# Kernel optimization log

Measured on AMD Instinct MI355X. Metric: run time of the kernel, lower is better.

The kernel has to match this reference:

```python
import jax, jax.numpy as jnp
import numpy as np

GAMMA = 2.0
ALPHA = 0.25
EPS = 1e-4
BETA = 1.0 / 9.0  # smooth-L1 transition point


def _make_boxes(key, shape, img, smin, smax):
    k1, k2 = jax.random.split(key)
    ctr = jax.random.uniform(k1, shape + (2,), minval=0.0, maxval=img)
    wh = jax.random.uniform(k2, shape + (2,), minval=smin, maxval=smax)
    return jnp.concatenate([ctr - 0.5 * wh, ctr + 0.5 * wh], axis=-1)


def setup_inputs() -> dict:
    B, N, C, M = 8, 65536, 80, 64
    key = jax.random.key(0)
    k1, k2, k3, k4, k5 = jax.random.split(key, 5)
    classifications = jax.random.uniform(k1, (B, N, C), minval=0.0, maxval=1.0, dtype=jnp.float32)
    regressions = jax.random.normal(k2, (B, N, 4), dtype=jnp.float32)
    anchors = _make_boxes(k3, (1, N), 512.0, 16.0, 128.0)
    gt_boxes = _make_boxes(k4, (B, M), 512.0, 32.0, 256.0)
    labels = jax.random.randint(k5, (B, M), 0, C).astype(jnp.float32)
    # mark last quarter of annotations as padding (label == -1), keep >=1 valid
    pad = jnp.arange(M) >= (3 * M // 4)
    labels = jnp.where(pad[None, :], -1.0, labels)
    annotations = jnp.concatenate([gt_boxes, labels[..., None]], axis=-1)
    return {"classifications": classifications, "regressions": regressions,
            "anchors": anchors, "annotations": annotations}


def _pairwise_iou(a, b):
    # a: (N,4), b: (M,4) boxes as (x1,y1,x2,y2) -> (N,M)
    area_a = (a[:, 2] - a[:, 0]) * (a[:, 3] - a[:, 1])
    area_b = (b[:, 2] - b[:, 0]) * (b[:, 3] - b[:, 1])
    iw = jnp.clip(jnp.minimum(a[:, None, 2], b[None, :, 2]) - jnp.maximum(a[:, None, 0], b[None, :, 0]), 0.0)
    ih = jnp.clip(jnp.minimum(a[:, None, 3], b[None, :, 3]) - jnp.maximum(a[:, None, 1], b[None, :, 1]), 0.0)
    inter = iw * ih
    ua = jnp.clip(area_a[:, None] + area_b[None, :] - inter, 1e-8)
    return inter / ua


def _focal_loss(classifications, regressions, anchors, annotations):
    anchor = anchors[0]  # (N,4)
    aw = anchor[:, 2] - anchor[:, 0]
    ah = anchor[:, 3] - anchor[:, 1]
    acx = anchor[:, 0] + 0.5 * aw
    acy = anchor[:, 1] + 0.5 * ah
    norm = jnp.array([0.1, 0.1, 0.2, 0.2], dtype=jnp.float32)

    def per_image(cls, reg, ann):
        labels = ann[:, 4]
        valid = labels != -1.0  # (M,)
        cls = jnp.clip(cls, EPS, 1.0 - EPS)  # (N,C)
        iou = _pairwise_iou(anchor, ann[:, :4])  # (N,M)
        iou = jnp.where(valid[None, :], iou, -1.0)  # exclude padded annotations
        iou_max = jnp.max(iou, axis=1)
        iou_argmax = jnp.argmax(iou, axis=1)
        pos = iou_max > 0.5
        neg = iou_max < 0.4
        num_pos = jnp.sum(pos.astype(jnp.float32))
        assigned = ann[iou_argmax]  # (N,5) gather of matched annotation
        one_hot = jax.nn.one_hot(assigned[:, 4].astype(jnp.int32), cls.shape[-1], dtype=cls.dtype)
        # -1 = ignore, 0 = background, one-hot for positives
        targets = jnp.where(pos[:, None], one_hot,
                            jnp.where(neg[:, None], 0.0, -1.0))
        alpha_f = jnp.where(targets == 1.0, ALPHA, 1.0 - ALPHA)
        fw = jnp.where(targets == 1.0, 1.0 - cls, cls)
        fw = alpha_f * fw ** GAMMA
        bce = -(targets * jnp.log(cls) + (1.0 - targets) * jnp.log(1.0 - cls))
        cls_loss = jnp.where(targets == -1.0, 0.0, fw * bce)
        cls_loss = jnp.sum(cls_loss) / jnp.maximum(num_pos, 1.0)
        gw = assigned[:, 2] - assigned[:, 0]
        gh = assigned[:, 3] - assigned[:, 1]
        gcx = assigned[:, 0] + 0.5 * gw
        gcy = assigned[:, 1] + 0.5 * gh
        gw = jnp.clip(gw, 1.0)
        gh = jnp.clip(gh, 1.0)
        t = jnp.stack([(gcx - acx) / aw, (gcy - acy) / ah,
                       jnp.log(gw / aw), jnp.log(gh / ah)], axis=1) / norm
        diff = jnp.abs(t - reg)
        sl1 = jnp.where(diff < BETA, 0.5 * 9.0 * diff ** 2, diff - 0.5 / 9.0)
        sl1 = jnp.where(pos[:, None], sl1, 0.0)
        reg_loss = jnp.where(num_pos > 0,
                             jnp.sum(sl1) / (jnp.maximum(num_pos, 1.0) * 4.0), 0.0)
        return cls_loss, reg_loss

    cls_losses, reg_losses = jax.vmap(per_image)(classifications, regressions, annotations)
    return jnp.mean(cls_losses) + jnp.mean(reg_losses)


def reference(classifications, regressions, anchors, annotations):
    return _focal_loss(classifications, regressions, anchors, annotations)
```

## Files before the change

kernel.cpp:

```cpp
#include <hip/hip_runtime.h>
#include <math.h>

constexpr int B = 8, N = 65536, C = 80, M = 64;
constexpr int APB = 256;
constexpr int BPI = N / APB;
constexpr float F_ALPHA = 0.25f;
constexpr float F_EPS = 1e-4f;
constexpr float F_BETA = 1.0f / 9.0f;
constexpr float K_NEG = 0.75f * 0.6931471805599453f;

__device__ __forceinline__ float waveReduceSum(float v) {
    #pragma unroll
    for (int off = 32; off > 0; off >>= 1) v += __shfl_down(v, off, 64);
    return v;
}

__global__ __launch_bounds__(256) void fused_kernel(
    const float* __restrict__ anchors,
    const float* __restrict__ regs,
    const float* __restrict__ ann,
    const float* __restrict__ cls,
    float4* __restrict__ partials)
{
    const int b = blockIdx.y;
    const int n0 = blockIdx.x * APB;
    const int tid = threadIdx.x;
    const int wave = tid >> 6, lane = tid & 63;

    __shared__ float4 sbox[M];
    __shared__ float  sarea[M];
    __shared__ float  slab[M];
    __shared__ float  slim[APB];
    __shared__ float  swsum[3][4];

    if (tid < M) {
        const float* a = ann + (size_t)(b * M + tid) * 5;
        const float x1 = a[0], y1 = a[1], x2 = a[2], y2 = a[3], lb = a[4];
        sbox[tid] = make_float4(x1, y1, x2, y2);
        sarea[tid] = (lb != -1.0f) ? (x2 - x1) * (y2 - y1) : __builtin_huge_valf();
        slab[tid] = lb;
    }
    __syncthreads();

    const int n = n0 + tid;
    const float4 av = reinterpret_cast<const float4*>(anchors)[n];
    const float aarea = (av.z - av.x) * (av.w - av.y);

    float bn = -1.0f, bd = 0.0f;
    int bestj = 0;
    #pragma unroll 8
    for (int j = 0; j < M; ++j) {
        const float4 bb = sbox[j];
        const float iw = fmaxf(fminf(av.z, bb.z) - fmaxf(av.x, bb.x), 0.0f);
        const float ih = fmaxf(fminf(av.w, bb.w) - fmaxf(av.y, bb.y), 0.0f);
        const float inter = iw * ih;
        const float ua = fmaxf(aarea + sarea[j] - inter, 1e-8f);
        const bool take = inter * bd > bn * ua;
        bn = take ? inter : bn;
        bd = take ? ua : bd;
        bestj = take ? j : bestj;
    }
    const bool pos = bn > 0.5f * bd;
    const bool neg = bn < 0.4f * bd;
    const int code = pos ? (int)slab[bestj] : (neg ? -2 : -1);
    slim[tid] = (pos || neg) ? (1.0f - F_EPS) : 0.0f;

    float np = 0.0f, rl = 0.0f, delta = 0.0f;
    if (pos) {
        np = 1.0f;
        const float4 g = sbox[bestj];
        float gw = g.z - g.x, gh = g.w - g.y;
        const float gcx = g.x + 0.5f * gw, gcy = g.y + 0.5f * gh;
        gw = fmaxf(gw, 1.0f);
        gh = fmaxf(gh, 1.0f);
        const float aw = av.z - av.x, ah = av.w - av.y;
        const float acx = av.x + 0.5f * aw, acy = av.y + 0.5f * ah;
        const float t0 = ((gcx - acx) / aw) / 0.1f;
        const float t1 = ((gcy - acy) / ah) / 0.1f;
        const float t2 = logf(gw / aw) / 0.2f;
        const float t3 = logf(gh / ah) / 0.2f;
        const float4 rv = reinterpret_cast<const float4*>(regs)[(size_t)b * N + n];
        const float d0 = fabsf(t0 - rv.x), d1 = fabsf(t1 - rv.y);
        const float d2 = fabsf(t2 - rv.z), d3 = fabsf(t3 - rv.w);
        auto sl1 = [](float d) { return d < F_BETA ? 4.5f * d * d : d - (0.5f / 9.0f); };
        rl = sl1(d0) + sl1(d1) + sl1(d2) + sl1(d3);

        const float xp = cls[((size_t)b * N + n) * C + code];
        const float x = fminf(fmaxf(xp, F_EPS), 1.0f - F_EPS);
        const float om = 1.0f - x;
        delta = F_ALPHA * om * om * (-__logf(x))
              - (1.0f - F_ALPHA) * x * x * (-__logf(om));
    }

    np = waveReduceSum(np);
    rl = waveReduceSum(rl);
    if (lane == 0) { swsum[0][wave] = np; swsum[1][wave] = rl; }
    __syncthreads();

    const float4* __restrict__ cp =
        reinterpret_cast<const float4*>(cls) + ((size_t)b * N + n0) * (C / 4);
    float a0 = 0.0f, a1 = 0.0f, a2 = 0.0f, a3 = 0.0f;
    #pragma unroll 4
    for (int k = 0; k < APB * C / 4 / 256; ++k) {
        const int f = k * 256 + tid;
        const int nl = f / 20;
        const float lim = slim[nl];
        const float4 v = cp[f];
        const float vv[4] = {v.x, v.y, v.z, v.w};
        float* accp[4] = {&a0, &a1, &a2, &a3};
        #pragma unroll
        for (int q = 0; q < 4; ++q) {
            const float x = fminf(vv[q], lim);
            *accp[q] = fmaf(x * x, __log2f(1.0f - x), *accp[q]);
        }
    }
    const float cl_t = fmaf(-K_NEG, (a0 + a1) + (a2 + a3), delta);
    float cl = waveReduceSum(cl_t);
    if (lane == 0) swsum[2][wave] = cl;
    __syncthreads();

    if (tid == 0) {
        float4 r;
        r.x = swsum[0][0] + swsum[0][1] + swsum[0][2] + swsum[0][3];
        r.y = swsum[1][0] + swsum[1][1] + swsum[1][2] + swsum[1][3];
        r.z = swsum[2][0] + swsum[2][1] + swsum[2][2] + swsum[2][3];
        r.w = 0.0f;
        partials[b * BPI + blockIdx.x] = r;
    }
}

__global__ __launch_bounds__(512) void final_kernel(
    const float4* __restrict__ partials, float* __restrict__ out)
{
    const int wave = threadIdx.x >> 6, lane = threadIdx.x & 63;
    __shared__ float simg[8];

    float np = 0.0f, rl = 0.0f, cl = 0.0f;
    for (int k = lane; k < BPI; k += 64) {
        const float4 p = partials[wave * BPI + k];
        np += p.x; rl += p.y; cl += p.z;
    }
    np = waveReduceSum(np);
    rl = waveReduceSum(rl);
    cl = waveReduceSum(cl);
    if (lane == 0) {
        const float c = cl / fmaxf(np, 1.0f);
        const float r = (np > 0.0f) ? rl / (fmaxf(np, 1.0f) * 4.0f) : 0.0f;
        simg[wave] = c + r;
    }
    __syncthreads();
    if (threadIdx.x == 0) {
        float t = 0.0f;
        #pragma unroll
        for (int b2 = 0; b2 < B; ++b2) t += simg[b2];
        out[0] = t * (1.0f / (float)B);
    }
}

extern "C" void kernel_launch(void* const* d_in, const int* in_sizes, int n_in,
                              void* d_out, int out_size, void* d_ws, size_t ws_size,
                              hipStream_t stream) {
    const float* classifications = (const float*)d_in[0];
    const float* regressions     = (const float*)d_in[1];
    const float* anchors         = (const float*)d_in[2];
    const float* annotations     = (const float*)d_in[3];
    float* out = (float*)d_out;
    float4* partials = (float4*)d_ws;

    dim3 g(BPI, B);
    fused_kernel<<<g, 256, 0, stream>>>(anchors, regressions, annotations,
                                        classifications, partials);
    final_kernel<<<1, 512, 0, stream>>>(partials, out);
}
```

Measured before the change: 37.58 us.

## Interleave IoU matching with unmasked class-loss streaming and correct ignored anchors afterward

The class-probability stream is now read and accumulated with a fixed clamp while the IoU argmax loop runs, so the memory loads overlap with the matching arithmetic. This removes the shared-memory per-anchor limit table and one barrier. Afterwards, ignored anchors re-read their own row and subtract its contribution, and positive anchors subtract their label term and add the alpha term. The cost is extra uncoalesced row reads for ignored anchors and a different floating-point summation order.

```diff
diff --git a/kernel.cpp b/kernel.cpp
--- a/kernel.cpp
+++ b/kernel.cpp
@@ -4,9 +4,11 @@
 constexpr int B = 8, N = 65536, C = 80, M = 64;
 constexpr int APB = 256;
 constexpr int BPI = N / APB;
+constexpr int K4 = C / 4;
 constexpr float F_ALPHA = 0.25f;
 constexpr float F_EPS = 1e-4f;
 constexpr float F_BETA = 1.0f / 9.0f;
+constexpr float F_LIM = 1.0f - F_EPS;
 constexpr float K_NEG = 0.75f * 0.6931471805599453f;
 
 __device__ __forceinline__ float waveReduceSum(float v) {
@@ -30,7 +32,6 @@
     __shared__ float4 sbox[M];
     __shared__ float  sarea[M];
     __shared__ float  slab[M];
-    __shared__ float  slim[APB];
     __shared__ float  swsum[3][4];
 
     if (tid < M) {
@@ -46,10 +47,14 @@
     const float4 av = reinterpret_cast<const float4*>(anchors)[n];
     const float aarea = (av.z - av.x) * (av.w - av.y);
 
+    const float4* __restrict__ cp =
+        reinterpret_cast<const float4*>(cls) + ((size_t)b * N + n0) * K4;
+
     float bn = -1.0f, bd = 0.0f;
     int bestj = 0;
-    #pragma unroll 8
-    for (int j = 0; j < M; ++j) {
+    float a0 = 0.0f, a1 = 0.0f, a2 = 0.0f, a3 = 0.0f;
+
+    auto iou_step = [&](int j) {
         const float4 bb = sbox[j];
         const float iw = fmaxf(fminf(av.z, bb.z) - fmaxf(av.x, bb.x), 0.0f);
         const float ih = fmaxf(fminf(av.w, bb.w) - fmaxf(av.y, bb.y), 0.0f);
@@ -59,13 +64,32 @@
         bn = take ? inter : bn;
         bd = take ? ua : bd;
         bestj = take ? j : bestj;
+    };
+
+    #pragma unroll 4
+    for (int k = 0; k < K4; ++k) {
+        const float4 v = cp[k * 256 + tid];
+        iou_step(3 * k);
+        iou_step(3 * k + 1);
+        iou_step(3 * k + 2);
+        const float vv[4] = {v.x, v.y, v.z, v.w};
+        float* accp[4] = {&a0, &a1, &a2, &a3};
+        #pragma unroll
+        for (int q = 0; q < 4; ++q) {
+            const float x = fminf(vv[q], F_LIM);
+            *accp[q] = fmaf(x * x, __log2f(1.0f - x), *accp[q]);
+        }
     }
+    #pragma unroll
+    for (int j = 60; j < 64; ++j) iou_step(j);
+
     const bool pos = bn > 0.5f * bd;
     const bool neg = bn < 0.4f * bd;
-    const int code = pos ? (int)slab[bestj] : (neg ? -2 : -1);
-    slim[tid] = (pos || neg) ? (1.0f - F_EPS) : 0.0f;
 
-    float np = 0.0f, rl = 0.0f, delta = 0.0f;
+    float np = 0.0f, rl = 0.0f;
+    float corr = 0.0f;
+    float posadd = 0.0f;
+
     if (pos) {
         np = 1.0f;
         const float4 g = sbox[bestj];
@@ -85,40 +109,38 @@
         auto sl1 = [](float d) { return d < F_BETA ? 4.5f * d * d : d - (0.5f / 9.0f); };
         rl = sl1(d0) + sl1(d1) + sl1(d2) + sl1(d3);
 
+        const int code = (int)slab[bestj];
         const float xp = cls[((size_t)b * N + n) * C + code];
-        const float x = fminf(fmaxf(xp, F_EPS), 1.0f - F_EPS);
-        const float om = 1.0f - x;
-        delta = F_ALPHA * om * om * (-__logf(x))
-              - (1.0f - F_ALPHA) * x * x * (-__logf(om));
+        const float xs = fminf(xp, F_LIM);
+        corr = xs * xs * __log2f(1.0f - xs);
+        const float xr = fminf(fmaxf(xp, F_EPS), F_LIM);
+        const float om = 1.0f - xr;
+        posadd = F_ALPHA * om * om * (-__logf(xr));
+    } else if (!neg) {
+        const float4* __restrict__ rowp =
+            reinterpret_cast<const float4*>(cls) + ((size_t)b * N + n) * K4;
+        float c0 = 0.0f, c1 = 0.0f, c2 = 0.0f, c3 = 0.0f;
+        #pragma unroll 4
+        for (int kk = 0; kk < K4; ++kk) {
+            const float4 w = rowp[kk];
+            const float ww[4] = {w.x, w.y, w.z, w.w};
+            float* ccp[4] = {&c0, &c1, &c2, &c3};
+            #pragma unroll
+            for (int q = 0; q < 4; ++q) {
+                const float x = fminf(ww[q], F_LIM);
+                *ccp[q] = fmaf(x * x, __log2f(1.0f - x), *ccp[q]);
+            }
+        }
+        corr = (c0 + c1) + (c2 + c3);
     }
+
+    const float cl_t = fmaf(-K_NEG, ((a0 + a1) + (a2 + a3)) - corr, posadd);
 
     np = waveReduceSum(np);
     rl = waveReduceSum(rl);
-    if (lane == 0) { swsum[0][wave] = np; swsum[1][wave] = rl; }
+    float cl = waveReduceSum(cl_t);
+    if (lane == 0) { swsum[0][wave] = np; swsum[1][wave] = rl; swsum[2][wave] = cl; }
     __syncthreads();
-
-    const float4* __restrict__ cp =
-        reinterpret_cast<const float4*>(cls) + ((size_t)b * N + n0) * (C / 4);
-    float a0 = 0.0f, a1 = 0.0f, a2 = 0.0f, a3 = 0.0f;
-    #pragma unroll 4
-    for (int k = 0; k < APB * C / 4 / 256; ++k) {
-        const int f = k * 256 + tid;
-        const int nl = f / 20;
-        const float lim = slim[nl];
-        const float4 v = cp[f];
-        const float vv[4] = {v.x, v.y, v.z, v.w};
-        float* accp[4] = {&a0, &a1, &a2, &a3};
-        #pragma unroll
-        for (int q = 0; q < 4; ++q) {
-            const float x = fminf(vv[q], lim);
-            *accp[q] = fmaf(x * x, __log2f(1.0f - x), *accp[q]);
-        }
-    }
-    const float cl_t = fmaf(-K_NEG, (a0 + a1) + (a2 + a3), delta);
-    float cl = waveReduceSum(cl_t);
-    if (lane == 0) swsum[2][wave] = cl;
-    __syncthreads();
-
     if (tid == 0) {
         float4 r;
         r.x = swsum[0][0] + swsum[0][1] + swsum[0][2] + swsum[0][3];
```

After: 43.67 us. 1.16x slower.

## Compact valid annotations, make classification pass wave-local, drop block barriers

Applied to the files above, without the earlier changes.

Valid ground-truth boxes are compacted with a ballot so the IoU loop runs only over valid boxes, padded to a multiple of eight, which skips the padded quarter. Each wave now streams the classification rows of its own 64 anchors and fetches the per-anchor clamp limit with a lane shuffle, so the shared slim array and the intermediate __syncthreads are gone. Per-wave partials are written straight to the workspace, which quadruples the number of partials the final kernel has to reduce. The IoU loop bound now depends on data, so it may unroll less well.

```diff
diff --git a/kernel.cpp b/kernel.cpp
--- a/kernel.cpp
+++ b/kernel.cpp
@@ -4,9 +4,11 @@
 constexpr int B = 8, N = 65536, C = 80, M = 64;
 constexpr int APB = 256;
 constexpr int BPI = N / APB;
+constexpr int K4 = C / 4;
 constexpr float F_ALPHA = 0.25f;
 constexpr float F_EPS = 1e-4f;
 constexpr float F_BETA = 1.0f / 9.0f;
+constexpr float F_LIM = 1.0f - F_EPS;
 constexpr float K_NEG = 0.75f * 0.6931471805599453f;
 
 __device__ __forceinline__ float waveReduceSum(float v) {
@@ -27,20 +29,32 @@
     const int tid = threadIdx.x;
     const int wave = tid >> 6, lane = tid & 63;
 
-    __shared__ float4 sbox[M];
-    __shared__ float  sarea[M];
-    __shared__ float  slab[M];
-    __shared__ float  slim[APB];
-    __shared__ float  swsum[3][4];
+    __shared__ float4 sbox[M + 8];
+    __shared__ float  sarea[M + 8];
+    __shared__ float  slab[M + 8];
+    __shared__ int    sMvPad;
 
     if (tid < M) {
         const float* a = ann + (size_t)(b * M + tid) * 5;
         const float x1 = a[0], y1 = a[1], x2 = a[2], y2 = a[3], lb = a[4];
-        sbox[tid] = make_float4(x1, y1, x2, y2);
-        sarea[tid] = (lb != -1.0f) ? (x2 - x1) * (y2 - y1) : __builtin_huge_valf();
-        slab[tid] = lb;
+        const bool valid = (lb != -1.0f);
+        const unsigned long long mask = __ballot(valid);
+        const int slot = __popcll(mask & ((1ull << lane) - 1ull));
+        const int Mv = __popcll(mask);
+        if (lane < 8) {
+            sbox[Mv + lane] = make_float4(0.f, 0.f, 0.f, 0.f);
+            sarea[Mv + lane] = __builtin_huge_valf();
+            slab[Mv + lane] = -1.0f;
+        }
+        if (valid) {
+            sbox[slot] = make_float4(x1, y1, x2, y2);
+            sarea[slot] = (x2 - x1) * (y2 - y1);
+            slab[slot] = lb;
+        }
+        if (lane == 0) sMvPad = (Mv + 7) & ~7;
     }
     __syncthreads();
+    const int MvPad = sMvPad;
 
     const int n = n0 + tid;
     const float4 av = reinterpret_cast<const float4*>(anchors)[n];
@@ -48,22 +62,24 @@
 
     float bn = -1.0f, bd = 0.0f;
     int bestj = 0;
-    #pragma unroll 8
-    for (int j = 0; j < M; ++j) {
-        const float4 bb = sbox[j];
-        const float iw = fmaxf(fminf(av.z, bb.z) - fmaxf(av.x, bb.x), 0.0f);
-        const float ih = fmaxf(fminf(av.w, bb.w) - fmaxf(av.y, bb.y), 0.0f);
-        const float inter = iw * ih;
-        const float ua = fmaxf(aarea + sarea[j] - inter, 1e-8f);
-        const bool take = inter * bd > bn * ua;
-        bn = take ? inter : bn;
-        bd = take ? ua : bd;
-        bestj = take ? j : bestj;
+    for (int j0 = 0; j0 < MvPad; j0 += 8) {
+        #pragma unroll
+        for (int u = 0; u < 8; ++u) {
+            const int j = j0 + u;
+            const float4 bb = sbox[j];
+            const float iw = fmaxf(fminf(av.z, bb.z) - fmaxf(av.x, bb.x), 0.0f);
+            const float ih = fmaxf(fminf(av.w, bb.w) - fmaxf(av.y, bb.y), 0.0f);
+            const float inter = iw * ih;
+            const float ua = fmaxf(aarea + sarea[j] - inter, 1e-8f);
+            const bool take = inter * bd > bn * ua;
+            bn = take ? inter : bn;
+            bd = take ? ua : bd;
+            bestj = take ? j : bestj;
+        }
     }
     const bool pos = bn > 0.5f * bd;
     const bool neg = bn < 0.4f * bd;
-    const int code = pos ? (int)slab[bestj] : (neg ? -2 : -1);
-    slim[tid] = (pos || neg) ? (1.0f - F_EPS) : 0.0f;
+    const float limf = (pos || neg) ? F_LIM : 0.0f;
 
     float np = 0.0f, rl = 0.0f, delta = 0.0f;
     if (pos) {
@@ -85,27 +101,23 @@
         auto sl1 = [](float d) { return d < F_BETA ? 4.5f * d * d : d - (0.5f / 9.0f); };
         rl = sl1(d0) + sl1(d1) + sl1(d2) + sl1(d3);
 
+        const int code = (int)slab[bestj];
         const float xp = cls[((size_t)b * N + n) * C + code];
-        const float x = fminf(fmaxf(xp, F_EPS), 1.0f - F_EPS);
+        const float x = fminf(fmaxf(xp, F_EPS), F_LIM);
         const float om = 1.0f - x;
         delta = F_ALPHA * om * om * (-__logf(x))
               - (1.0f - F_ALPHA) * x * x * (-__logf(om));
     }
 
-    np = waveReduceSum(np);
-    rl = waveReduceSum(rl);
-    if (lane == 0) { swsum[0][wave] = np; swsum[1][wave] = rl; }
-    __syncthreads();
-
-    const float4* __restrict__ cp =
-        reinterpret_cast<const float4*>(cls) + ((size_t)b * N + n0) * (C / 4);
+    const float4* __restrict__ cpw =
+        reinterpret_cast<const float4*>(cls) + ((size_t)b * N + n0 + wave * 64) * K4;
     float a0 = 0.0f, a1 = 0.0f, a2 = 0.0f, a3 = 0.0f;
     #pragma unroll 4
-    for (int k = 0; k < APB * C / 4 / 256; ++k) {
-        const int f = k * 256 + tid;
+    for (int k = 0; k < K4; ++k) {
+        const int f = k * 64 + lane;
         const int nl = f / 20;
-        const float lim = slim[nl];
-        const float4 v = cp[f];
+        const float lim = __shfl(limf, nl, 64);
+        const float4 v = cpw[f];
         const float vv[4] = {v.x, v.y, v.z, v.w};
         float* accp[4] = {&a0, &a1, &a2, &a3};
         #pragma unroll
@@ -115,17 +127,13 @@
         }
     }
     const float cl_t = fmaf(-K_NEG, (a0 + a1) + (a2 + a3), delta);
+
+    np = waveReduceSum(np);
+    rl = waveReduceSum(rl);
     float cl = waveReduceSum(cl_t);
-    if (lane == 0) swsum[2][wave] = cl;
-    __syncthreads();
-
-    if (tid == 0) {
-        float4 r;
-        r.x = swsum[0][0] + swsum[0][1] + swsum[0][2] + swsum[0][3];
-        r.y = swsum[1][0] + swsum[1][1] + swsum[1][2] + swsum[1][3];
-        r.z = swsum[2][0] + swsum[2][1] + swsum[2][2] + swsum[2][3];
-        r.w = 0.0f;
-        partials[b * BPI + blockIdx.x] = r;
+    if (lane == 0) {
+        partials[(((size_t)b * BPI + blockIdx.x) << 2) | wave] =
+            make_float4(np, rl, cl, 0.0f);
     }
 }
 
@@ -134,10 +142,11 @@
 {
     const int wave = threadIdx.x >> 6, lane = threadIdx.x & 63;
     __shared__ float simg[8];
+    constexpr int PPI = BPI * 4;
 
     float np = 0.0f, rl = 0.0f, cl = 0.0f;
-    for (int k = lane; k < BPI; k += 64) {
-        const float4 p = partials[wave * BPI + k];
+    for (int k = lane; k < PPI; k += 64) {
+        const float4 p = partials[wave * PPI + k];
         np += p.x; rl += p.y; cl += p.z;
     }
     np = waveReduceSum(np);
```

Result: no change. 38.20 us (+1.6%).
